# Optimization experiments

Hardware: AMD Instinct MI355X
Metric: run time of the kernel (lower is better)

The kernel has to match this reference:

```python
import jax, jax.numpy as jnp
import numpy as np

LOG_2PI = float(np.log(2.0 * np.pi))


def gaussian_log_density(samples, mean, log_squared_scale):
    inv_sigma = jnp.exp(-log_squared_scale)
    tmp = samples - mean
    return -0.5 * (tmp * tmp * inv_sigma + log_squared_scale + LOG_2PI)


def setup_inputs() -> dict:
    key = jax.random.key(0)
    k1, k2, k3, k4, k5 = jax.random.split(key, 5)
    B, L, D = 4096, 16, 512
    return {
        "data": jax.random.normal(k1, (B, D), dtype=jnp.float32),
        "reconstruction": jax.random.normal(k2, (B, D), dtype=jnp.float32),
        "z": jax.random.normal(k3, (B, L), dtype=jnp.float32),
        "z_mean": jax.random.normal(k4, (B, L), dtype=jnp.float32),
        "z_log_var": jax.random.normal(k5, (B, L), dtype=jnp.float32),
    }


def reference(data, reconstruction, z, z_mean, z_log_var):
    # reconstruction loss: mean over batch of per-sample MAE (mean over feature axis)
    recon_loss = jnp.mean(jnp.abs(data - reconstruction))

    # KL penalty: mean over batch of 0.5 * sum over latents
    summand = jnp.square(z_mean) + jnp.exp(z_log_var) - z_log_var - 1.0
    kl_loss = jnp.mean(0.5 * jnp.sum(summand, axis=1))

    # total correlation: pairwise gaussian log-density [B, B, L]
    log_qz_prob = gaussian_log_density(
        z[:, None, :], z_mean[None, :, :], z_log_var[None, :, :]
    )
    # log prod_l q(z_l): logsumexp over batch axis 1 per latent, then sum over latents
    log_qz_product = jnp.sum(jax.nn.logsumexp(log_qz_prob, axis=1), axis=1)
    # log q(z): sum over latents first, then logsumexp over batch axis
    log_qz = jax.nn.logsumexp(jnp.sum(log_qz_prob, axis=2), axis=1)
    tc_loss = jnp.mean(log_qz - log_qz_product)

    total_loss = recon_loss + kl_loss + tc_loss
    return total_loss
```

## Files before the change

kernel.cpp:

```cpp
#include <hip/hip_runtime.h>
#include <hip/hip_fp16.h>
#include <math.h>

#define BB 4096
#define LL 16
#define DD 512

#define NPTS   1024
#define XMIN   -6.0f
#define XRANGE 12.0f

#define LOG2E_F  1.4426950408889634f
#define LN2_F    0.6931471805599453f
#define LOG2PI_F 1.8378770664093453f

#define OFFC     22.942540f
#define SCALE23  8388608.0f
#define BIASF    126.94269504f

#if __has_builtin(__builtin_amdgcn_exp2f)
#define EXP2(x) __builtin_amdgcn_exp2f(x)
#else
#define EXP2(x) exp2f(x)
#endif
#if __has_builtin(__builtin_amdgcn_logf)
#define LOG2(x) __builtin_amdgcn_logf(x)
#else
#define LOG2(x) log2f(x)
#endif

typedef float f32x2 __attribute__((ext_vector_type(2)));

#define CJ_F   0
#define CT_F   147456
#define RP_F   344064
#define KLP_F  346112
#define TP_F   346368
#define TAB_F  870656
#define JP_F   887040

__device__ __forceinline__ float block_reduce(float v) {
  __shared__ float sm[4];
  __syncthreads();
#pragma unroll
  for (int off = 32; off; off >>= 1) v += __shfl_xor(v, off);
  if ((threadIdx.x & 63) == 0) sm[threadIdx.x >> 6] = v;
  __syncthreads();
  if (threadIdx.x == 0) v = (sm[0] + sm[1]) + (sm[2] + sm[3]);
  return v;
}

__global__ __launch_bounds__(256) void prep_recon_kernel(
    const float4* __restrict__ data4, const float4* __restrict__ recon4,
    const float* __restrict__ zm, const float* __restrict__ zlv,
    float* __restrict__ cj, float* __restrict__ ct,
    float* __restrict__ rp, float* __restrict__ klp,
    float* __restrict__ out) {
  const int tid = threadIdx.x;
  const int b = blockIdx.x;

  if (b == 1024 && tid == 0) out[0] = 0.0f;

  {
    const int n4 = (BB * DD) / 4;
    int stride = gridDim.x * 256;
    float s = 0.0f;
    for (int k = b * 256 + tid; k < n4; k += stride) {
      float4 a = data4[k];
      float4 r = recon4[k];
      s += (fabsf(a.x - r.x) + fabsf(a.y - r.y)) +
           (fabsf(a.z - r.z) + fabsf(a.w - r.w));
    }
    float t = block_reduce(s);
    if (tid == 0) rp[b] = t * (1.0f / (float)(BB * DD));
  }

  if (b < 256) {
    const float S = 1024.0f / 65535.0f;
    int idx = b * 256 + tid;
    int j = idx >> 4;
    int l = idx & 15;
    float m = zm[idx];
    float lv = zlv[idx];
    float inv = EXP2(-lv * LOG2E_F);
    float a = -0.5f * LOG2E_F * inv;
    float c2 = -0.5f * LOG2E_F * (lv + LOG2PI_F);
    float braw = -2.0f * a * m;
    float craw = fmaf(a, m * m, c2);

    cj[j * 36 + l]      = a * S;
    cj[j * 36 + 16 + l] = braw * S;
    float cs = (craw + OFFC) * S;
    cs += __shfl_xor(cs, 1); cs += __shfl_xor(cs, 2);
    cs += __shfl_xor(cs, 4); cs += __shfl_xor(cs, 8);
    if (l == 0) cj[j * 36 + 32] = cs;

    ct[(0 * 16 + l) * 4096 + j] = a;
    ct[(1 * 16 + l) * 4096 + j] = braw;
    ct[(2 * 16 + l) * 4096 + j] = craw;

    float kls = m * m + EXP2(lv * LOG2E_F) - lv - 1.0f;
    float s = block_reduce(kls);
    if (tid == 0) klp[b] = s * (0.5f / (float)BB);
  }
}

__global__ __launch_bounds__(256) void table_build(
    const float* __restrict__ ct, float* __restrict__ tpart) {
  __shared__ float la[128], lb[128], lc[128];
  const int tid = threadIdx.x;
  const int jc = blockIdx.x;
  const int l  = blockIdx.y;
  const int j0 = jc * 128;
  if (tid < 128) {
    la[tid] = ct[(0 * 16 + l) * 4096 + j0 + tid];
    lb[tid] = ct[(1 * 16 + l) * 4096 + j0 + tid];
    lc[tid] = ct[(2 * 16 + l) * 4096 + j0 + tid];
  }
  const float H = XRANGE / (float)(NPTS - 1);
  float x[4], acc[4];
#pragma unroll
  for (int k = 0; k < 4; ++k) {
    x[k] = XMIN + (float)(k * 256 + tid) * H;
    acc[k] = 0.0f;
  }
  __syncthreads();
#pragma unroll 2
  for (int j = 0; j < 128; ++j) {
    float a = la[j], b = lb[j], c = lc[j];
#pragma unroll
    for (int k = 0; k < 4; ++k) {
      float lp = fmaf(fmaf(a, x[k], b), x[k], c);
      acc[k] += EXP2(lp);
    }
  }
  float* o = tpart + ((size_t)jc * 16 + l) * NPTS;
#pragma unroll
  for (int k = 0; k < 4; ++k) o[k * 256 + tid] = acc[k];
}

__global__ __launch_bounds__(256) void table_reduce(
    const float* __restrict__ tpart, float* __restrict__ table) {
  const int e = blockIdx.x * 256 + threadIdx.x;
  float s = 0.0f;
#pragma unroll 4
  for (int jc = 0; jc < 32; ++jc) s += tpart[(size_t)jc * (16 * NPTS) + e];
  table[e] = s;
}

template <int CHUNK, int R>
__global__ __launch_bounds__(256, 2) void tc_joint(
    const float* __restrict__ z, const float* __restrict__ cj,
    float* __restrict__ jp) {
  __shared__ float lcj[CHUNK * 36];
  const int tid = threadIdx.x;
  const int i0 = blockIdx.x * (256 * R) + tid;
  const int j0 = blockIdx.y * CHUNK;
  const float JMUL = 65535.0f * 8192.0f;
  const float JK   = -SCALE23 * (16.0f * OFFC - BIASF);

  {
    const float4* g4 = (const float4*)(cj + (size_t)j0 * 36);
    float4* l4 = (float4*)lcj;
    for (int t = tid; t < (CHUNK * 36) / 4; t += 256) l4[t] = g4[t];
  }

  f32x2 zv[R][8];
#pragma unroll
  for (int r = 0; r < R; ++r) {
    const float4* zp = (const float4*)(z + (size_t)(i0 + 256 * r) * 16);
#pragma unroll
    for (int q = 0; q < 4; ++q) {
      float4 v = zp[q];
      zv[r][2 * q]     = (f32x2){v.x, v.y};
      zv[r][2 * q + 1] = (f32x2){v.z, v.w};
    }
  }
#pragma unroll
  for (int r = 0; r < R; ++r)
#pragma unroll
    for (int p = 0; p < 8; ++p) asm volatile("" : "+v"(zv[r][p]));

  float accJ[R];
#pragma unroll
  for (int r = 0; r < R; ++r) accJ[r] = 0.0f;

  __syncthreads();

#pragma unroll 2
  for (int j = 0; j < CHUNK; ++j) {
    const float* cp = lcj + j * 36;
    f32x2 A[8], Bv[8];
#pragma unroll
    for (int t = 0; t < 4; ++t) {
      *(float4*)&A[2 * t]  = *(const float4*)(cp + 4 * t);
      *(float4*)&Bv[2 * t] = *(const float4*)(cp + 16 + 4 * t);
    }
    float Cs = cp[32];
#pragma unroll
    for (int r = 0; r < R; ++r) {
      f32x2 acc = (f32x2){0.0f, 0.0f};
#pragma unroll
      for (int p = 0; p < 8; ++p) {
        f32x2 t2 = __builtin_elementwise_fma(A[p], zv[r][p], Bv[p]);
        acc = __builtin_elementwise_fma(t2, zv[r][p], acc);
      }
      float js = (acc.x + acc.y) + Cs;
      float w = fmaf(js, JMUL, JK);
      unsigned u;
      asm("v_cvt_u32_f32 %0, %1" : "=v"(u) : "v"(w));
      accJ[r] += __uint_as_float(u);
    }
  }

#pragma unroll
  for (int r = 0; r < R; ++r)
    jp[(size_t)blockIdx.y * BB + (size_t)(i0 + 256 * r)] = accJ[r];
}

__global__ __launch_bounds__(256) void final_kernel(
    const float* __restrict__ z, const float* __restrict__ jp,
    const float* __restrict__ table, const float* __restrict__ rp,
    const float* __restrict__ klp, float* __restrict__ out, int nc) {
  __shared__ float ltab[16 * NPTS];
  const int tid = threadIdx.x;
  const int i = blockIdx.x * 256 + tid;

  for (int t = tid; t < 16 * NPTS; t += 256) ltab[t] = table[t];

  float s0 = 0.0f, s1 = 0.0f, s2 = 0.0f, s3 = 0.0f;
  for (int c = 0; c < nc; c += 4) {
    s0 += jp[(size_t)(c + 0) * BB + i];
    s1 += jp[(size_t)(c + 1) * BB + i];
    s2 += jp[(size_t)(c + 2) * BB + i];
    s3 += jp[(size_t)(c + 3) * BB + i];
  }
  float lg = LOG2((s0 + s1) + (s2 + s3));

  __syncthreads();

  const float4* zp = (const float4*)(z + (size_t)i * 16);
  const float SC = (float)(NPTS - 1) / XRANGE;
#pragma unroll
  for (int q = 0; q < 4; ++q) {
    float4 v = zp[q];
    float xs[4] = {v.x, v.y, v.z, v.w};
#pragma unroll
    for (int k = 0; k < 4; ++k) {
      int l = 4 * q + k;
      float t = (xs[k] - XMIN) * SC;
      t = fminf(fmaxf(t, 0.0f), (float)(NPTS - 2) + 0.999f);
      int g = (int)t;
      float f = t - (float)g;
      float m0 = ltab[l * NPTS + g];
      float m1 = ltab[l * NPTS + g + 1];
      lg -= LOG2(fmaf(f, m1 - m0, m0));
    }
  }

  float tval = lg * (LN2_F / (float)BB);
  if (blockIdx.x == 0) {
#pragma unroll
    for (int q = 0; q < 8; ++q) tval += rp[tid + 256 * q];
    tval += klp[tid];
  }

  __syncthreads();
#pragma unroll
  for (int off = 32; off; off >>= 1) tval += __shfl_xor(tval, off);
  if ((tid & 63) == 0) ltab[tid >> 6] = tval;
  __syncthreads();
  if (tid == 0) atomicAdd(out, (ltab[0] + ltab[1]) + (ltab[2] + ltab[3]));
}

extern "C" void kernel_launch(void* const* d_in, const int* in_sizes, int n_in,
                              void* d_out, int out_size, void* d_ws, size_t ws_size,
                              hipStream_t stream) {
  const float* data  = (const float*)d_in[0];
  const float* recon = (const float*)d_in[1];
  const float* z     = (const float*)d_in[2];
  const float* zm    = (const float*)d_in[3];
  const float* zlv   = (const float*)d_in[4];
  float* out = (float*)d_out;
  float* ws  = (float*)d_ws;

  const int nc = 128;

  float* cj   = ws + CJ_F;
  float* ct   = ws + CT_F;
  float* rp   = ws + RP_F;
  float* klp  = ws + KLP_F;
  float* tp   = ws + TP_F;
  float* tab  = ws + TAB_F;
  float* jp   = ws + JP_F;

  hipLaunchKernelGGL(prep_recon_kernel, dim3(2048), dim3(256), 0, stream,
                     reinterpret_cast<const float4*>(data),
                     reinterpret_cast<const float4*>(recon),
                     zm, zlv, cj, ct, rp, klp, out);
  hipLaunchKernelGGL(table_build, dim3(32, 16), dim3(256), 0, stream,
                     ct, tp);
  hipLaunchKernelGGL(table_reduce, dim3((16 * NPTS) / 256), dim3(256), 0,
                     stream, tp, tab);
  hipLaunchKernelGGL((tc_joint<32, 4>), dim3(4, 128), dim3(256), 0, stream,
                     z, cj, jp);
  hipLaunchKernelGGL(final_kernel, dim3(BB / 256), dim3(256), 0, stream,
                     z, jp, tab, rp, klp, out, nc);
}
```

Measured before the change: 119.1 us.

## Compute pairwise joint log-density with bf16 split-precision MFMA matrix multiply

Recasts the per-pair quadratic sum over latents as a K=128 dot product between per-j coefficient rows (a, b, c split into bf16 hi/lo parts) and per-i feature rows (x^2, x, 1 split into hi/lo), computed with 32x32x16 bf16 MFMA instructions instead of packed FP32 FMAs. The prep kernel now also builds the split feature matrix from z. The exp2 via integer-convert trick then runs on the MFMA accumulators, and the number of j-chunk partial sums drops from 128 to 32. This trades exactness for bf16x2 split precision, and it drops the old offset constant, so the u32 conversion may overflow or underflow for extreme values.

After: 114.4 us. 3.9% less time.

```diff
diff --git a/kernel.cpp b/kernel.cpp
--- a/kernel.cpp
+++ b/kernel.cpp
@@ -14,7 +14,6 @@
 #define LN2_F    0.6931471805599453f
 #define LOG2PI_F 1.8378770664093453f
 
-#define OFFC     22.942540f
 #define SCALE23  8388608.0f
 #define BIASF    126.94269504f
 
@@ -29,15 +28,28 @@
 #define LOG2(x) log2f(x)
 #endif
 
-typedef float f32x2 __attribute__((ext_vector_type(2)));
-
-#define CJ_F   0
-#define CT_F   147456
-#define RP_F   344064
-#define KLP_F  346112
-#define TP_F   346368
-#define TAB_F  870656
-#define JP_F   887040
+typedef short bf16x8 __attribute__((ext_vector_type(8)));
+typedef unsigned short u16x8 __attribute__((ext_vector_type(8)));
+typedef float f32x16 __attribute__((ext_vector_type(16)));
+
+#define WM_F   0
+#define FM_F   262144
+#define CT_F   524288
+#define RP_F   720896
+#define KLP_F  722944
+#define TP_F   723200
+#define TAB_F  1247488
+#define JP_F   1263872
+
+__device__ __forceinline__ void split_bf16(float x, unsigned short& h,
+                                           unsigned short& l) {
+  unsigned u = __float_as_uint(x);
+  h = (unsigned short)(u >> 16);
+  float hf = __uint_as_float((unsigned)h << 16);
+  unsigned v = __float_as_uint(x - hf);
+  unsigned r = v + 0x7FFFu + ((v >> 16) & 1u);
+  l = (unsigned short)(r >> 16);
+}
 
 __device__ __forceinline__ float block_reduce(float v) {
   __shared__ float sm[4];
@@ -53,9 +65,10 @@
 __global__ __launch_bounds__(256) void prep_recon_kernel(
     const float4* __restrict__ data4, const float4* __restrict__ recon4,
     const float* __restrict__ zm, const float* __restrict__ zlv,
-    float* __restrict__ cj, float* __restrict__ ct,
-    float* __restrict__ rp, float* __restrict__ klp,
-    float* __restrict__ out) {
+    const float* __restrict__ z,
+    unsigned short* __restrict__ Wm, unsigned short* __restrict__ Fm,
+    float* __restrict__ ct, float* __restrict__ rp,
+    float* __restrict__ klp, float* __restrict__ out) {
   const int tid = threadIdx.x;
   const int b = blockIdx.x;
 
@@ -76,7 +89,6 @@
   }
 
   if (b < 256) {
-    const float S = 1024.0f / 65535.0f;
     int idx = b * 256 + tid;
     int j = idx >> 4;
     int l = idx & 15;
@@ -88,12 +100,12 @@
     float braw = -2.0f * a * m;
     float craw = fmaf(a, m * m, c2);
 
-    cj[j * 36 + l]      = a * S;
-    cj[j * 36 + 16 + l] = braw * S;
-    float cs = (craw + OFFC) * S;
-    cs += __shfl_xor(cs, 1); cs += __shfl_xor(cs, 2);
-    cs += __shfl_xor(cs, 4); cs += __shfl_xor(cs, 8);
-    if (l == 0) cj[j * 36 + 32] = cs;
+    unsigned short Ah, Al, Bh, Bl, Ch, Cl;
+    split_bf16(a, Ah, Al);
+    split_bf16(braw, Bh, Bl);
+    split_bf16(craw, Ch, Cl);
+    u16x8 wv8 = {Ah, Ah, Al, Bh, Bh, Bl, Ch, Cl};
+    *(u16x8*)(Wm + (size_t)j * 128 + 8 * l) = wv8;
 
     ct[(0 * 16 + l) * 4096 + j] = a;
     ct[(1 * 16 + l) * 4096 + j] = braw;
@@ -102,6 +114,17 @@
     float kls = m * m + EXP2(lv * LOG2E_F) - lv - 1.0f;
     float s = block_reduce(kls);
     if (tid == 0) klp[b] = s * (0.5f / (float)BB);
+  } else if (b < 512) {
+    int idx = (b - 256) * 256 + tid;
+    int i = idx >> 4;
+    int l = idx & 15;
+    float x = z[idx];
+    float x2 = x * x;
+    unsigned short x2h, x2l, xh, xl;
+    split_bf16(x2, x2h, x2l);
+    split_bf16(x, xh, xl);
+    u16x8 fv8 = {x2h, x2l, x2h, xh, xl, xh, 0x3F80, 0x3F80};
+    *(u16x8*)(Fm + (size_t)i * 128 + 8 * l) = fv8;
   }
 }
 
@@ -127,10 +150,10 @@
   __syncthreads();
 #pragma unroll 2
   for (int j = 0; j < 128; ++j) {
-    float a = la[j], b = lb[j], c = lc[j];
+    float a = la[j], bb = lb[j], c = lc[j];
 #pragma unroll
     for (int k = 0; k < 4; ++k) {
-      float lp = fmaf(fmaf(a, x[k], b), x[k], c);
+      float lp = fmaf(fmaf(a, x[k], bb), x[k], c);
       acc[k] += EXP2(lp);
     }
   }
@@ -148,80 +171,57 @@
   table[e] = s;
 }
 
-template <int CHUNK, int R>
-__global__ __launch_bounds__(256, 2) void tc_joint(
-    const float* __restrict__ z, const float* __restrict__ cj,
-    float* __restrict__ jp) {
-  __shared__ float lcj[CHUNK * 36];
+__global__ __launch_bounds__(256, 4) void mfma_joint(
+    const unsigned short* __restrict__ Wm,
+    const unsigned short* __restrict__ Fm, float* __restrict__ jp) {
   const int tid = threadIdx.x;
-  const int i0 = blockIdx.x * (256 * R) + tid;
-  const int j0 = blockIdx.y * CHUNK;
-  const float JMUL = 65535.0f * 8192.0f;
-  const float JK   = -SCALE23 * (16.0f * OFFC - BIASF);
-
-  {
-    const float4* g4 = (const float4*)(cj + (size_t)j0 * 36);
-    float4* l4 = (float4*)lcj;
-    for (int t = tid; t < (CHUNK * 36) / 4; t += 256) l4[t] = g4[t];
-  }
-
-  f32x2 zv[R][8];
-#pragma unroll
-  for (int r = 0; r < R; ++r) {
-    const float4* zp = (const float4*)(z + (size_t)(i0 + 256 * r) * 16);
-#pragma unroll
-    for (int q = 0; q < 4; ++q) {
-      float4 v = zp[q];
-      zv[r][2 * q]     = (f32x2){v.x, v.y};
-      zv[r][2 * q + 1] = (f32x2){v.z, v.w};
-    }
-  }
-#pragma unroll
-  for (int r = 0; r < R; ++r)
-#pragma unroll
-    for (int p = 0; p < 8; ++p) asm volatile("" : "+v"(zv[r][p]));
-
-  float accJ[R];
-#pragma unroll
-  for (int r = 0; r < R; ++r) accJ[r] = 0.0f;
-
-  __syncthreads();
-
-#pragma unroll 2
-  for (int j = 0; j < CHUNK; ++j) {
-    const float* cp = lcj + j * 36;
-    f32x2 A[8], Bv[8];
-#pragma unroll
-    for (int t = 0; t < 4; ++t) {
-      *(float4*)&A[2 * t]  = *(const float4*)(cp + 4 * t);
-      *(float4*)&Bv[2 * t] = *(const float4*)(cp + 16 + 4 * t);
-    }
-    float Cs = cp[32];
-#pragma unroll
-    for (int r = 0; r < R; ++r) {
-      f32x2 acc = (f32x2){0.0f, 0.0f};
-#pragma unroll
-      for (int p = 0; p < 8; ++p) {
-        f32x2 t2 = __builtin_elementwise_fma(A[p], zv[r][p], Bv[p]);
-        acc = __builtin_elementwise_fma(t2, zv[r][p], acc);
-      }
-      float js = (acc.x + acc.y) + Cs;
-      float w = fmaf(js, JMUL, JK);
+  const int lane = tid & 63;
+  const int wv = tid >> 6;
+  const int i0 = blockIdx.x * 128 + wv * 32;
+  const int jt0 = blockIdx.y * 4;
+  const int r32 = lane & 31;
+  const int khalf = (lane >> 5) * 8;
+
+  bf16x8 bfr[8];
+  const unsigned short* frow = Fm + (size_t)(i0 + r32) * 128 + khalf;
+#pragma unroll
+  for (int s = 0; s < 8; ++s) bfr[s] = *(const bf16x8*)(frow + 16 * s);
+#pragma unroll
+  for (int s = 0; s < 8; ++s) asm volatile("" : "+v"(bfr[s]));
+
+  const float KK = SCALE23 * BIASF;
+  float accJ = 0.0f;
+
+#pragma unroll
+  for (int t = 0; t < 4; ++t) {
+    const int j0 = (jt0 + t) * 32;
+    const unsigned short* wrow = Wm + (size_t)(j0 + r32) * 128 + khalf;
+    f32x16 acc;
+#pragma unroll
+    for (int e = 0; e < 16; ++e) acc[e] = 0.0f;
+#pragma unroll
+    for (int s = 0; s < 8; ++s) {
+      bf16x8 af = *(const bf16x8*)(wrow + 16 * s);
+      acc = __builtin_amdgcn_mfma_f32_32x32x16_bf16(af, bfr[s], acc, 0, 0, 0);
+    }
+#pragma unroll
+    for (int e = 0; e < 16; ++e) {
+      float w = fmaf(acc[e], SCALE23, KK);
       unsigned u;
       asm("v_cvt_u32_f32 %0, %1" : "=v"(u) : "v"(w));
-      accJ[r] += __uint_as_float(u);
-    }
-  }
-
-#pragma unroll
-  for (int r = 0; r < R; ++r)
-    jp[(size_t)blockIdx.y * BB + (size_t)(i0 + 256 * r)] = accJ[r];
+      accJ += __uint_as_float(u);
+    }
+  }
+
+  accJ += __shfl_xor(accJ, 32);
+  if (lane < 32)
+    jp[(size_t)blockIdx.y * BB + (size_t)(i0 + r32)] = accJ;
 }
 
 __global__ __launch_bounds__(256) void final_kernel(
     const float* __restrict__ z, const float* __restrict__ jp,
     const float* __restrict__ table, const float* __restrict__ rp,
-    const float* __restrict__ klp, float* __restrict__ out, int nc) {
+    const float* __restrict__ klp, float* __restrict__ out) {
   __shared__ float ltab[16 * NPTS];
   const int tid = threadIdx.x;
   const int i = blockIdx.x * 256 + tid;
@@ -229,7 +229,8 @@
   for (int t = tid; t < 16 * NPTS; t += 256) ltab[t] = table[t];
 
   float s0 = 0.0f, s1 = 0.0f, s2 = 0.0f, s3 = 0.0f;
-  for (int c = 0; c < nc; c += 4) {
+#pragma unroll 8
+  for (int c = 0; c < 32; c += 4) {
     s0 += jp[(size_t)(c + 0) * BB + i];
     s1 += jp[(size_t)(c + 1) * BB + i];
     s2 += jp[(size_t)(c + 2) * BB + i];
@@ -284,26 +285,25 @@
   float* out = (float*)d_out;
   float* ws  = (float*)d_ws;
 
-  const int nc = 128;
-
-  float* cj   = ws + CJ_F;
-  float* ct   = ws + CT_F;
-  float* rp   = ws + RP_F;
-  float* klp  = ws + KLP_F;
-  float* tp   = ws + TP_F;
-  float* tab  = ws + TAB_F;
-  float* jp   = ws + JP_F;
+  unsigned short* Wm = (unsigned short*)(ws + WM_F);
+  unsigned short* Fm = (unsigned short*)(ws + FM_F);
+  float* ct  = ws + CT_F;
+  float* rp  = ws + RP_F;
+  float* klp = ws + KLP_F;
+  float* tp  = ws + TP_F;
+  float* tab = ws + TAB_F;
+  float* jp  = ws + JP_F;
 
   hipLaunchKernelGGL(prep_recon_kernel, dim3(2048), dim3(256), 0, stream,
                      reinterpret_cast<const float4*>(data),
                      reinterpret_cast<const float4*>(recon),
-                     zm, zlv, cj, ct, rp, klp, out);
+                     zm, zlv, z, Wm, Fm, ct, rp, klp, out);
   hipLaunchKernelGGL(table_build, dim3(32, 16), dim3(256), 0, stream,
                      ct, tp);
   hipLaunchKernelGGL(table_reduce, dim3((16 * NPTS) / 256), dim3(256), 0,
                      stream, tp, tab);
-  hipLaunchKernelGGL((tc_joint<32, 4>), dim3(4, 128), dim3(256), 0, stream,
-                     z, cj, jp);
+  hipLaunchKernelGGL(mfma_joint, dim3(32, 32), dim3(256), 0, stream,
+                     Wm, Fm, jp);
   hipLaunchKernelGGL(final_kernel, dim3(BB / 256), dim3(256), 0, stream,
-                     z, jp, tab, rp, klp, out, nc);
-}
+                     z, jp, tab, rp, klp, out);
+}
```
